# Performance work log

Hardware: AMD Instinct MI355X
Metric: run time of the kernel (lower is better)

## Reference

```python
import jax, jax.numpy as jnp
import numpy as np

DIM = 512
HEADS = 8
EPS = 1e-12  # matches torch F.normalize default eps


def setup_inputs() -> dict:
    key = jax.random.key(0)
    k1, k2, k3, k4 = jax.random.split(key, 4)
    x = jax.random.normal(k1, (4, 2048, DIM), dtype=jnp.float32)
    # nn.Linear(dim, dim*3, bias=False): weight [3*dim, dim], y = x @ W.T
    w_qkv = jax.random.normal(k2, (3 * DIM, DIM), dtype=jnp.float32) * (1.0 / np.sqrt(DIM))
    w_out = jax.random.normal(k3, (DIM, DIM), dtype=jnp.float32) * (1.0 / np.sqrt(DIM))
    temperature = jnp.ones((HEADS, 1, 1), dtype=jnp.float32)
    return {"x": x, "w_qkv": w_qkv, "w_out": w_out, "temperature": temperature}


def _l2norm(t):
    # torch F.normalize(dim=-1): t / max(||t||, eps)
    n = jnp.sqrt(jnp.sum(t * t, axis=-1, keepdims=True))
    return t / jnp.maximum(n, EPS)


def reference(x, w_qkv, w_out, temperature):
    b, n, c = x.shape
    h = HEADS
    d = c // h
    qkv = x @ w_qkv.T  # [b, n, 3c]
    qkv = qkv.reshape(b, n, 3, h, d).transpose(2, 0, 3, 1, 4)  # [3, b, h, n, d]
    q, k, v = qkv[0], qkv[1], qkv[2]
    q = _l2norm(q)
    k = _l2norm(k)
    # cosine attention with learned per-head temperature
    attn = jnp.einsum("bhnd,bhmd->bhnm", q, k) * temperature  # temp broadcasts [h,1,1]
    attn = jax.nn.softmax(attn, axis=-1)
    out = jnp.einsum("bhnm,bhmd->bhnd", attn, v)  # [b, h, n, d]
    out = out.transpose(0, 2, 1, 3).reshape(b, n, c)
    return out @ w_out.T
```

## Files before the change

### kernel.cpp

```cpp
#include <hip/hip_runtime.h>
#include <hip/hip_bf16.h>

using bf16x8 = __attribute__((ext_vector_type(8))) short;
using f32x4  = __attribute__((ext_vector_type(4))) float;
using f32x16 = __attribute__((ext_vector_type(16))) float;
using u32x4  = __attribute__((ext_vector_type(4))) unsigned;

__device__ __forceinline__ short f2bf(float f) {
  union { float f; unsigned u; } v; v.f = f;
  unsigned r = (v.u + 0x7FFFu + ((v.u >> 16) & 1u)) >> 16;
  return (short)(unsigned short)r;
}

__device__ __forceinline__ unsigned cvtpk(float lo, float hi) {
  unsigned r;
  asm("v_cvt_pk_bf16_f32 %0, %1, %2" : "=v"(r) : "v"(lo), "v"(hi));
  return r;
}

__device__ __forceinline__ void plswap(unsigned &a, unsigned &b) {
  asm("v_permlane32_swap_b32 %0, %1" : "+v"(a), "+v"(b));
}

#define GLLDS(gp, lp) __builtin_amdgcn_global_load_lds(                        \
    (const __attribute__((address_space(1))) void*)(gp),                       \
    (__attribute__((address_space(3))) void*)(lp), 16, 0, 0)

__global__ __launch_bounds__(256)
void cvt_f32_bf16(const float* __restrict__ in, short* __restrict__ out, int n8)
{
  int i = blockIdx.x * 256 + threadIdx.x;
  if (i >= n8) return;
  float4 lo = *(const float4*)(in + (size_t)i * 8);
  float4 hi = *(const float4*)(in + (size_t)i * 8 + 4);
  uint4 r;
  r.x = cvtpk(lo.x, lo.y);
  r.y = cvtpk(lo.z, lo.w);
  r.z = cvtpk(hi.x, hi.y);
  r.w = cvtpk(hi.z, hi.w);
  *(uint4*)(out + (size_t)i * 8) = r;
}

__global__ __launch_bounds__(256, 2)
void gemm_qkv(const short* __restrict__ A, const short* __restrict__ B,
              short* __restrict__ outQ, short* __restrict__ outK,
              short* __restrict__ outVt, const float* __restrict__ temp)
{
  __shared__ short As[128 * 32];
  __shared__ short Bs[128 * 32];
  const int Kd = 512;
  const int tid  = threadIdx.x;
  const int lane = tid & 63;
  const int w    = tid >> 6;
  const int wr   = w >> 1, wc = w & 1;
  const int fr   = lane & 15, fq = lane >> 4;
  const int bm = blockIdx.y, bn = blockIdx.x;
  const int rowA = bm * 128, rowB = bn * 128;

  const int lrow   = lane >> 2;
  const int lchunk = ((lane & 3) ^ ((lane >> 3) & 3)) * 8;
  const short* gA0 = A + (size_t)(rowA + w * 32 + lrow) * Kd + lchunk;
  const short* gB0 = B + (size_t)(rowB + w * 32 + lrow) * Kd + lchunk;
  char* lA0 = (char*)As + (w * 32) * 64;
  char* lB0 = (char*)Bs + (w * 32) * 64;
  const int rxor = ((fr >> 1) & 3) << 4;

  f32x4 acc[4][4];
  #pragma unroll
  for (int m = 0; m < 4; ++m)
    #pragma unroll
    for (int n = 0; n < 4; ++n) acc[m][n] = (f32x4){0.f, 0.f, 0.f, 0.f};

  for (int k0 = 0; k0 < Kd; k0 += 32) {
    GLLDS(gA0 + k0,            lA0);
    GLLDS(gA0 + k0 + 16 * Kd,  lA0 + 1024);
    GLLDS(gB0 + k0,            lB0);
    GLLDS(gB0 + k0 + 16 * Kd,  lB0 + 1024);
    __syncthreads();
    bf16x8 afr[4], bfr[4];
    #pragma unroll
    for (int m = 0; m < 4; ++m)
      afr[m] = *(const bf16x8*)((char*)As + (wr*64 + m*16 + fr) * 64 + ((fq*16) ^ rxor));
    #pragma unroll
    for (int n = 0; n < 4; ++n)
      bfr[n] = *(const bf16x8*)((char*)Bs + (wc*64 + n*16 + fr) * 64 + ((fq*16) ^ rxor));
    #pragma unroll
    for (int m = 0; m < 4; ++m)
      #pragma unroll
      for (int n = 0; n < 4; ++n)
        acc[m][n] = __builtin_amdgcn_mfma_f32_16x16x32_bf16(afr[m], bfr[n], acc[m][n], 0, 0, 0);
    __syncthreads();
  }

  const int gc0   = rowB + wc*64;
  const int slice = gc0 >> 6;
  const int t3    = slice >> 3;
  const int h     = slice & 7;
  if (t3 < 2) {
    float scl[4][4];
    const float tval = (t3 == 0) ? temp[h] * 1.44269504088896f : 1.0f;
    #pragma unroll
    for (int m = 0; m < 4; ++m) {
      #pragma unroll
      for (int r = 0; r < 4; ++r) {
        float ss = 0.f;
        #pragma unroll
        for (int n = 0; n < 4; ++n) ss += acc[m][n][r] * acc[m][n][r];
        #pragma unroll
        for (int off = 1; off < 16; off <<= 1) ss += __shfl_xor(ss, off);
        scl[m][r] = tval / fmaxf(sqrtf(ss), 1e-12f);
      }
    }
    short* dst = (t3 == 0) ? outQ : outK;
    #pragma unroll
    for (int m = 0; m < 4; ++m) {
      #pragma unroll
      for (int r = 0; r < 4; ++r) {
        int rg = rowA + wr*64 + m*16 + fq*4 + r;
        int b = rg >> 11, nn = rg & 2047;
        size_t rowoff = ((size_t)(b*8 + h) * 2048 + nn) * 64;
        #pragma unroll
        for (int n = 0; n < 4; ++n)
          dst[rowoff + n*16 + fr] = f2bf(acc[m][n][r] * scl[m][r]);
      }
    }
  } else {
    #pragma unroll
    for (int m = 0; m < 4; ++m) {
      #pragma unroll
      for (int r = 0; r < 4; ++r) {
        int rg = rowA + wr*64 + m*16 + fq*4 + r;
        int b = rg >> 11, nn = rg & 2047;
        #pragma unroll
        for (int n = 0; n < 4; ++n)
          outVt[((size_t)(b*8 + h) * 64 + n*16 + fr) * 2048 + nn] = f2bf(acc[m][n][r]);
      }
    }
  }
}

__global__ __launch_bounds__(256, 2)
void gemm_out(const short* __restrict__ A, const short* __restrict__ B,
              float* __restrict__ outC)
{
  __shared__ short As[128 * 32];
  __shared__ short Bs[128 * 32];
  const int Kd = 512, N = 512;
  const int tid  = threadIdx.x;
  const int lane = tid & 63;
  const int w    = tid >> 6;
  const int wr   = w >> 1, wc = w & 1;
  const int fr   = lane & 15, fq = lane >> 4;
  const int bm = blockIdx.y, bn = blockIdx.x;
  const int rowA = bm * 128, rowB = bn * 128;

  const int lrow   = lane >> 2;
  const int lchunk = ((lane & 3) ^ ((lane >> 3) & 3)) * 8;
  const short* gA0 = A + (size_t)(rowA + w * 32 + lrow) * Kd + lchunk;
  const short* gB0 = B + (size_t)(rowB + w * 32 + lrow) * Kd + lchunk;
  char* lA0 = (char*)As + (w * 32) * 64;
  char* lB0 = (char*)Bs + (w * 32) * 64;
  const int rxor = ((fr >> 1) & 3) << 4;

  f32x4 acc[4][4];
  #pragma unroll
  for (int m = 0; m < 4; ++m)
    #pragma unroll
    for (int n = 0; n < 4; ++n) acc[m][n] = (f32x4){0.f, 0.f, 0.f, 0.f};

  for (int k0 = 0; k0 < Kd; k0 += 32) {
    GLLDS(gA0 + k0,            lA0);
    GLLDS(gA0 + k0 + 16 * Kd,  lA0 + 1024);
    GLLDS(gB0 + k0,            lB0);
    GLLDS(gB0 + k0 + 16 * Kd,  lB0 + 1024);
    __syncthreads();
    bf16x8 afr[4], bfr[4];
    #pragma unroll
    for (int m = 0; m < 4; ++m)
      afr[m] = *(const bf16x8*)((char*)As + (wr*64 + m*16 + fr) * 64 + ((fq*16) ^ rxor));
    #pragma unroll
    for (int n = 0; n < 4; ++n)
      bfr[n] = *(const bf16x8*)((char*)Bs + (wc*64 + n*16 + fr) * 64 + ((fq*16) ^ rxor));
    #pragma unroll
    for (int m = 0; m < 4; ++m)
      #pragma unroll
      for (int n = 0; n < 4; ++n)
        acc[m][n] = __builtin_amdgcn_mfma_f32_16x16x32_bf16(afr[m], bfr[n], acc[m][n], 0, 0, 0);
    __syncthreads();
  }

  #pragma unroll
  for (int m = 0; m < 4; ++m) {
    int r0 = rowA + wr*64 + m*16 + fq*4;
    #pragma unroll
    for (int n = 0; n < 4; ++n) {
      int c = rowB + wc*64 + n*16 + fr;
      #pragma unroll
      for (int r = 0; r < 4; ++r)
        outC[(size_t)(r0 + r) * N + c] = acc[m][n][r];
    }
  }
}

__global__ __launch_bounds__(256, 2)
void attn_fwd(const short* __restrict__ Q, const short* __restrict__ Kt,
              const short* __restrict__ Vt, short* __restrict__ AO,
              const float* __restrict__ temp)
{
  __shared__ short Kl[2][64 * 64];
  __shared__ short Vl[2][64 * 64];
  __shared__ float Ls[4][32];
  const int tid  = threadIdx.x;
  const int lane = tid & 63;
  const int w    = tid >> 6;
  const int l31  = lane & 31;
  const int hi   = lane >> 5;
  const int bh = blockIdx.x;
  const int qt = blockIdx.y;
  const int b = bh >> 3, h = bh & 7;
  const size_t base  = (size_t)bh * 2048 * 64;
  const size_t vbase = (size_t)bh * 64 * 2048;
  const int q0 = qt * 128 + w * 32;

  const short* kp = Kt + base;
  const short* vp = Vt + vbase;

  const int srow  = tid >> 3;
  const int scol8 = (tid & 7) * 8;
  const int scolB = (tid & 7) * 16;
  const int sxor  = (srow & 7) << 4;
  const int kswz  = (l31 & 7) << 4;

  bf16x8 stK[2], stV[2];
  #define LOAD_TILE(T)                                                              \
    do { int kt_ = (T) * 64;                                                        \
      stK[0] = *(const bf16x8*)(kp + (size_t)(kt_ + srow)      * 64 + scol8);       \
      stK[1] = *(const bf16x8*)(kp + (size_t)(kt_ + 32 + srow) * 64 + scol8);       \
      stV[0] = *(const bf16x8*)(vp + (size_t)srow        * 2048 + kt_ + scol8);     \
      stV[1] = *(const bf16x8*)(vp + (size_t)(32 + srow) * 2048 + kt_ + scol8);     \
    } while (0)
  #define WRITE_TILE(P_)                                                            \
    do {                                                                            \
      *(bf16x8*)((char*)Kl[P_] + (srow)      * 128 + (scolB ^ sxor)) = stK[0];      \
      *(bf16x8*)((char*)Kl[P_] + (32 + srow) * 128 + (scolB ^ sxor)) = stK[1];      \
      *(bf16x8*)((char*)Vl[P_] + (srow)      * 128 + (scolB ^ sxor)) = stV[0];      \
      *(bf16x8*)((char*)Vl[P_] + (32 + srow) * 128 + (scolB ^ sxor)) = stV[1];      \
    } while (0)

  bf16x8 bq[4];
  #pragma unroll
  for (int dj = 0; dj < 4; ++dj)
    bq[dj] = *(const bf16x8*)(Q + base + (size_t)(q0 + l31) * 64 + dj*16 + hi*8);

  const float Mh = fabsf(temp[h]) * 1.44269504088896f;
  f32x16 cinit;
  #pragma unroll
  for (int r = 0; r < 16; ++r) cinit[r] = -Mh;

  f32x16 o[2];
  #pragma unroll
  for (int td = 0; td < 2; ++td)
    #pragma unroll
    for (int r = 0; r < 16; ++r) o[td][r] = 0.f;
  float lp = 0.f;

  LOAD_TILE(0); WRITE_TILE(0);
  LOAD_TILE(1); WRITE_TILE(1);
  LOAD_TILE(2);
  __syncthreads();

  for (int t = 0; t < 32; ++t) {
    const int p = t & 1;
    const char* kl = (const char*)Kl[p];
    const char* vl = (const char*)Vl[p];

    f32x16 s[2];
    #pragma unroll
    for (int tk = 0; tk < 2; ++tk) {
      f32x16 z = cinit;
      #pragma unroll
      for (int dj = 0; dj < 4; ++dj) {
        bf16x8 ak = *(const bf16x8*)(kl + (tk*32 + l31) * 128 + ((dj*32 + hi*16) ^ kswz));
        z = __builtin_amdgcn_mfma_f32_32x32x16_bf16(ak, bq[dj], z, 0, 0, 0);
      }
      s[tk] = z;
    }
    #pragma unroll
    for (int tk = 0; tk < 2; ++tk)
      #pragma unroll
      for (int r = 0; r < 16; ++r) {
        float pv = __builtin_amdgcn_exp2f(s[tk][r]);
        s[tk][r] = pv;
        lp += pv;
      }
    bf16x8 pa[4];
    #pragma unroll
    for (int tk = 0; tk < 2; ++tk)
      #pragma unroll
      for (int j = 0; j < 2; ++j) {
        unsigned w0 = cvtpk(s[tk][8*j+0], s[tk][8*j+1]);
        unsigned w2 = cvtpk(s[tk][8*j+4], s[tk][8*j+5]);
        unsigned w1 = cvtpk(s[tk][8*j+2], s[tk][8*j+3]);
        unsigned w3 = cvtpk(s[tk][8*j+6], s[tk][8*j+7]);
        plswap(w0, w2);
        plswap(w1, w3);
        u32x4 pw = {w0, w1, w2, w3};
        pa[tk*2 + j] = __builtin_bit_cast(bf16x8, pw);
      }
    #pragma unroll
    for (int td = 0; td < 2; ++td) {
      f32x16 acc = o[td];
      #pragma unroll
      for (int kj = 0; kj < 4; ++kj) {
        bf16x8 bv = *(const bf16x8*)(vl + (td*32 + l31) * 128 + ((kj*32 + hi*16) ^ kswz));
        acc = __builtin_amdgcn_mfma_f32_32x32x16_bf16(pa[kj], bv, acc, 0, 0, 0);
      }
      o[td] = acc;
    }

    if (t < 31) {
      __syncthreads();
      if (t < 30) {
        WRITE_TILE(p);
        if (t < 29) LOAD_TILE(t + 3);
      }
    }
  }
  #undef LOAD_TILE
  #undef WRITE_TILE

  lp += __shfl_xor(lp, 32);
  if (hi == 0) Ls[w][l31] = 1.0f / lp;
  #pragma unroll
  for (int td = 0; td < 2; ++td)
    #pragma unroll
    for (int r = 0; r < 16; ++r) {
      int qr = (r & 3) + 8 * (r >> 2) + 4 * hi;
      float li = Ls[w][qr];
      int row = b * 2048 + q0 + qr;
      int col = h * 64 + td * 32 + l31;
      AO[(size_t)row * 512 + col] = f2bf(o[td][r] * li);
    }
}

extern "C" void kernel_launch(void* const* d_in, const int* in_sizes, int n_in,
                              void* d_out, int out_size, void* d_ws, size_t ws_size,
                              hipStream_t stream)
{
  const float* x     = (const float*)d_in[0];
  const float* w_qkv = (const float*)d_in[1];
  const float* w_out = (const float*)d_in[2];
  const float* temp  = (const float*)d_in[3];
  float* out = (float*)d_out;
  short* ws  = (short*)d_ws;

  const size_t NQ = (size_t)4 * 8 * 2048 * 64;
  short* Qb   = ws;
  short* Kb   = ws + NQ;
  short* Vtb  = ws + 2 * NQ;
  short* AO16 = ws + 3 * NQ;
  short* xb   = ws + 4 * NQ;
  short* wb   = AO16;
  short* wob  = xb;

  cvt_f32_bf16<<<dim3(2048), 256, 0, stream>>>(x, xb, 524288);
  cvt_f32_bf16<<<dim3(384),  256, 0, stream>>>(w_qkv, wb, 98304);
  gemm_qkv<<<dim3(12, 64), 256, 0, stream>>>(xb, wb, Qb, Kb, Vtb, temp);
  cvt_f32_bf16<<<dim3(128),  256, 0, stream>>>(w_out, wob, 32768);
  attn_fwd<<<dim3(32, 16), 256, 0, stream>>>(Qb, Kb, Vtb, AO16, temp);
  gemm_out<<<dim3(4, 64), 256, 0, stream>>>(AO16, wob, out);
}
```

Baseline: 94.48 us.

## Merge input conversions, shrink gemm_out tile, add setprio around attention MFMAs

Merges the x and w_qkv fp32-to-bf16 conversions into one launch, removing a kernel launch. Changes gemm_out to a 128x64 tile with each wave owning 32 rows, which doubles the block count (256 to 512) for better CU occupancy on the small output GEMM, at the cost of less B-tile reuse per block. Wraps the QK and PV MFMA blocks in attn_fwd with s_setprio so waves issuing matrix ops get priority over others doing softmax or loads.

```diff
diff --git a/kernel.cpp b/kernel.cpp
--- a/kernel.cpp
+++ b/kernel.cpp
@@ -25,6 +25,26 @@
 #define GLLDS(gp, lp) __builtin_amdgcn_global_load_lds(                        \
     (const __attribute__((address_space(1))) void*)(gp),                       \
     (__attribute__((address_space(3))) void*)(lp), 16, 0, 0)
+
+__global__ __launch_bounds__(256)
+void cvt_xw(const float* __restrict__ x, const float* __restrict__ wq,
+            short* __restrict__ xb, short* __restrict__ wb)
+{
+  const int blk = blockIdx.x;
+  const float* src;
+  short* dst;
+  int i;
+  if (blk < 2048) { src = x;  dst = xb; i = blk * 256 + threadIdx.x; }
+  else            { src = wq; dst = wb; i = (blk - 2048) * 256 + threadIdx.x; }
+  float4 lo = *(const float4*)(src + (size_t)i * 8);
+  float4 hi = *(const float4*)(src + (size_t)i * 8 + 4);
+  uint4 r;
+  r.x = cvtpk(lo.x, lo.y);
+  r.y = cvtpk(lo.z, lo.w);
+  r.z = cvtpk(hi.x, hi.y);
+  r.w = cvtpk(hi.z, hi.w);
+  *(uint4*)(dst + (size_t)i * 8) = r;
+}
 
 __global__ __launch_bounds__(256)
 void cvt_f32_bf16(const float* __restrict__ in, short* __restrict__ out, int n8)
@@ -144,27 +164,26 @@
               float* __restrict__ outC)
 {
   __shared__ short As[128 * 32];
-  __shared__ short Bs[128 * 32];
+  __shared__ short Bs[64 * 32];
   const int Kd = 512, N = 512;
   const int tid  = threadIdx.x;
   const int lane = tid & 63;
   const int w    = tid >> 6;
-  const int wr   = w >> 1, wc = w & 1;
   const int fr   = lane & 15, fq = lane >> 4;
   const int bm = blockIdx.y, bn = blockIdx.x;
-  const int rowA = bm * 128, rowB = bn * 128;
+  const int rowA = bm * 128, rowB = bn * 64;
 
   const int lrow   = lane >> 2;
   const int lchunk = ((lane & 3) ^ ((lane >> 3) & 3)) * 8;
   const short* gA0 = A + (size_t)(rowA + w * 32 + lrow) * Kd + lchunk;
-  const short* gB0 = B + (size_t)(rowB + w * 32 + lrow) * Kd + lchunk;
+  const short* gB0 = B + (size_t)(rowB + w * 16 + lrow) * Kd + lchunk;
   char* lA0 = (char*)As + (w * 32) * 64;
-  char* lB0 = (char*)Bs + (w * 32) * 64;
+  char* lB0 = (char*)Bs + (w * 16) * 64;
   const int rxor = ((fr >> 1) & 3) << 4;
 
-  f32x4 acc[4][4];
-  #pragma unroll
-  for (int m = 0; m < 4; ++m)
+  f32x4 acc[2][4];
+  #pragma unroll
+  for (int m = 0; m < 2; ++m)
     #pragma unroll
     for (int n = 0; n < 4; ++n) acc[m][n] = (f32x4){0.f, 0.f, 0.f, 0.f};
 
@@ -172,17 +191,16 @@
     GLLDS(gA0 + k0,            lA0);
     GLLDS(gA0 + k0 + 16 * Kd,  lA0 + 1024);
     GLLDS(gB0 + k0,            lB0);
-    GLLDS(gB0 + k0 + 16 * Kd,  lB0 + 1024);
     __syncthreads();
-    bf16x8 afr[4], bfr[4];
-    #pragma unroll
-    for (int m = 0; m < 4; ++m)
-      afr[m] = *(const bf16x8*)((char*)As + (wr*64 + m*16 + fr) * 64 + ((fq*16) ^ rxor));
+    bf16x8 afr[2], bfr[4];
+    #pragma unroll
+    for (int m = 0; m < 2; ++m)
+      afr[m] = *(const bf16x8*)((char*)As + (w*32 + m*16 + fr) * 64 + ((fq*16) ^ rxor));
     #pragma unroll
     for (int n = 0; n < 4; ++n)
-      bfr[n] = *(const bf16x8*)((char*)Bs + (wc*64 + n*16 + fr) * 64 + ((fq*16) ^ rxor));
-    #pragma unroll
-    for (int m = 0; m < 4; ++m)
+      bfr[n] = *(const bf16x8*)((char*)Bs + (n*16 + fr) * 64 + ((fq*16) ^ rxor));
+    #pragma unroll
+    for (int m = 0; m < 2; ++m)
       #pragma unroll
       for (int n = 0; n < 4; ++n)
         acc[m][n] = __builtin_amdgcn_mfma_f32_16x16x32_bf16(afr[m], bfr[n], acc[m][n], 0, 0, 0);
@@ -190,11 +208,11 @@
   }
 
   #pragma unroll
-  for (int m = 0; m < 4; ++m) {
-    int r0 = rowA + wr*64 + m*16 + fq*4;
+  for (int m = 0; m < 2; ++m) {
+    int r0 = rowA + w*32 + m*16 + fq*4;
     #pragma unroll
     for (int n = 0; n < 4; ++n) {
-      int c = rowB + wc*64 + n*16 + fr;
+      int c = rowB + n*16 + fr;
       #pragma unroll
       for (int r = 0; r < 4; ++r)
         outC[(size_t)(r0 + r) * N + c] = acc[m][n][r];
@@ -275,6 +293,7 @@
     const char* vl = (const char*)Vl[p];
 
     f32x16 s[2];
+    __builtin_amdgcn_s_setprio(1);
     #pragma unroll
     for (int tk = 0; tk < 2; ++tk) {
       f32x16 z = cinit;
@@ -285,6 +304,7 @@
       }
       s[tk] = z;
     }
+    __builtin_amdgcn_s_setprio(0);
     #pragma unroll
     for (int tk = 0; tk < 2; ++tk)
       #pragma unroll
@@ -307,6 +327,7 @@
         u32x4 pw = {w0, w1, w2, w3};
         pa[tk*2 + j] = __builtin_bit_cast(bf16x8, pw);
       }
+    __builtin_amdgcn_s_setprio(1);
     #pragma unroll
     for (int td = 0; td < 2; ++td) {
       f32x16 acc = o[td];
@@ -317,6 +338,7 @@
       }
       o[td] = acc;
     }
+    __builtin_amdgcn_s_setprio(0);
 
     if (t < 31) {
       __syncthreads();
@@ -363,10 +385,9 @@
   short* wb   = AO16;
   short* wob  = xb;
 
-  cvt_f32_bf16<<<dim3(2048), 256, 0, stream>>>(x, xb, 524288);
-  cvt_f32_bf16<<<dim3(384),  256, 0, stream>>>(w_qkv, wb, 98304);
+  cvt_xw<<<dim3(2432), 256, 0, stream>>>(x, w_qkv, xb, wb);
   gemm_qkv<<<dim3(12, 64), 256, 0, stream>>>(xb, wb, Qb, Kb, Vtb, temp);
-  cvt_f32_bf16<<<dim3(128),  256, 0, stream>>>(w_out, wob, 32768);
+  cvt_f32_bf16<<<dim3(128), 256, 0, stream>>>(w_out, wob, 32768);
   attn_fwd<<<dim3(32, 16), 256, 0, stream>>>(Qb, Kb, Vtb, AO16, temp);
-  gemm_out<<<dim3(4, 64), 256, 0, stream>>>(AO16, wob, out);
-}
+  gemm_out<<<dim3(8, 64), 256, 0, stream>>>(AO16, wob, out);
+}
```

Result: no change. 92.81 us (-1.8%).
